# Optimization experiments

Measured on AMD Instinct MI355X. Metric: run time of the kernel, lower is better.

## Reference

```python
import jax, jax.numpy as jnp
import numpy as np

EPS = 1e-12  # torch F.normalize eps


def setup_inputs() -> dict:
    key = jax.random.key(0)
    k1, k2, k3 = jax.random.split(key, 3)
    B, C, N, E, EMB = 128, 16, 128, 4, 16
    OUT = EMB // E  # Linear(emb_sz, emb_sz // num_edges)
    x = jax.random.normal(k1, (B, C, N, EMB), dtype=jnp.float32)
    A = jax.random.uniform(k2, (E, N, N), dtype=jnp.float32)  # non-negative adjacency
    # per-edge-type Linear weights, stored [E, in, out] so y = x @ W[e]
    W = jax.random.normal(k3, (E, EMB, OUT), dtype=jnp.float32) * (1.0 / np.sqrt(EMB))
    return {"x": x, "A": A, "W": W}


def reference(x, A, W):
    # F.normalize(A[e], dim=0): L2-normalize each column -> norm over rows (axis=1 of [E,N,N])
    col_norm = jnp.sqrt(jnp.sum(A * A, axis=1, keepdims=True))  # [E,1,N]
    An = A / jnp.maximum(col_norm, EPS)                         # [E,N,N]
    # x.transpose(3,2) @ An[e] then transpose back:
    # out[e,b,c,m,f] = sum_n x[b,c,n,f] * An[e,n,m]
    msg = jnp.einsum('bcnf,enm->ebcmf', x, An)                  # [E,B,C,N,EMB]
    # per-edge Linear (bias=False) + relu
    h = jax.nn.relu(jnp.einsum('ebcmf,efo->ebcmo', msg, W))     # [E,B,C,N,OUT]
    E_, B, C, N, O = h.shape
    # torch.cat([h_0, h_1, ...], axis=1) -> [B, E*C, N, OUT]
    out = jnp.transpose(h, (1, 0, 2, 3, 4)).reshape(B, E_ * C, N, O)
    return out
```

## Files before the change

kernel.cpp:

```cpp
#include <hip/hip_runtime.h>
#include <math.h>

#define EPSN 1e-12f

typedef __attribute__((ext_vector_type(8))) __bf16 bf16x8;
typedef __attribute__((ext_vector_type(8))) short short8;
typedef __attribute__((ext_vector_type(4))) float floatx4;

static __device__ __forceinline__ unsigned short f2bf(float f) {
    return __builtin_bit_cast(unsigned short, (__bf16)f);
}

__global__ __launch_bounds__(512, 2)
void gcn_one(const float* __restrict__ x, const float* __restrict__ A,
             const float* __restrict__ W, float* __restrict__ out) {
    __shared__ __align__(16) unsigned char xw[32768];
    __shared__ __align__(16) unsigned char at[32768];
    __shared__ float red[16][128];

    const int t   = threadIdx.x;
    const int bc0 = blockIdx.x * 8;
    const int w   = t >> 6;
    const int l   = t & 63;
    const int cl  = l & 15;
    const int lg  = l >> 4;
    const int mw  = w * 16 + cl;
    const int mq  = t & 31;
    const int ng  = t >> 5;

    float4 v4[8];
    #pragma unroll
    for (int j = 0; j < 8; ++j)
        v4[j] = *(const float4*)(A + (size_t)(ng * 8 + j) * 128 + mq * 4);

    bf16x8 bW;
    {
        short8 z = {0, 0, 0, 0, 0, 0, 0, 0};
        bW = __builtin_bit_cast(bf16x8, z);
        if (lg < 2) {
            unsigned short hs[8] __attribute__((aligned(16)));
            #pragma unroll
            for (int j = 0; j < 8; ++j)
                hs[j] = f2bf(W[(cl >> 2) * 64 + (lg * 8 + j) * 4 + (cl & 3)]);
            bW = __builtin_bit_cast(bf16x8, *(const short8*)hs);
        }
    }
    #pragma unroll
    for (int ti = 0; ti < 8; ++ti) {
        int T = w * 8 + ti;
        bf16x8 ax;
        { short8 z = {0, 0, 0, 0, 0, 0, 0, 0}; ax = __builtin_bit_cast(bf16x8, z); }
        if (lg < 2) {
            int R = T * 16 + cl;
            const float* xp = x + ((size_t)bc0 * 128 + R) * 16 + lg * 8;
            float4 a = *(const float4*)xp;
            float4 b = *(const float4*)(xp + 4);
            unsigned short hs[8] __attribute__((aligned(16)));
            hs[0] = f2bf(a.x); hs[1] = f2bf(a.y); hs[2] = f2bf(a.z); hs[3] = f2bf(a.w);
            hs[4] = f2bf(b.x); hs[5] = f2bf(b.y); hs[6] = f2bf(b.z); hs[7] = f2bf(b.w);
            ax = __builtin_bit_cast(bf16x8, *(const short8*)hs);
        }
        floatx4 d = {0.f, 0.f, 0.f, 0.f};
        d = __builtin_amdgcn_mfma_f32_16x16x32_bf16(ax, bW, d, 0, 0, 0);
        int eD = cl >> 2, oD = cl & 3;
        int bcl = T >> 3;
        int nb  = (T & 7) * 16 + lg * 4;
        int r   = bcl * 4 + oD;
        int base = (eD * 32 + r) << 8;
        int s    = (r & 7) << 4;
        #pragma unroll
        for (int q = 0; q < 4; ++q) {
            int off = (base + (nb + q) * 2) ^ s;
            *(unsigned short*)(xw + off) = f2bf(d[q]);
        }
    }

    {
        floatx4 rs = {0.f, 0.f, 0.f, 0.f};
        #pragma unroll
        for (int i = 0; i < 4; ++i) {
            int m = mq * 4 + i;
            unsigned short hs[8] __attribute__((aligned(16)));
            #pragma unroll
            for (int j = 0; j < 8; ++j) {
                float vv = ((const float*)&v4[j])[i];
                rs[i] += vv * vv;
                hs[j] = f2bf(vv);
            }
            int slot = ng ^ (mq & 7);
            *(short8*)(at + ((m << 8) | (slot << 4))) = *(const short8*)hs;
        }
        *(float4*)&red[ng][mq * 4] = *(const float4*)&rs;
    }
    __syncthreads();

    #pragma unroll 1
    for (int e = 0; e < 4; ++e) {
        if (e < 3) {
            const float* An = A + (size_t)(e + 1) * 16384;
            #pragma unroll
            for (int j = 0; j < 8; ++j)
                v4[j] = *(const float4*)(An + (size_t)(ng * 8 + j) * 128 + mq * 4);
        }
        bf16x8 af[2][4];
        #pragma unroll
        for (int rt = 0; rt < 2; ++rt)
            #pragma unroll
            for (int ks = 0; ks < 4; ++ks) {
                int row = rt * 16 + cl;
                int off = (((e * 32 + row) << 8) + (ks * 32 + lg * 8) * 2)
                          ^ ((row & 7) << 4);
                af[rt][ks] = __builtin_bit_cast(bf16x8, *(const short8*)(xw + off));
            }
        bf16x8 bfr[4];
        #pragma unroll
        for (int ks = 0; ks < 4; ++ks) {
            int slot = (ks * 4 + lg) ^ ((mw >> 2) & 7);
            bfr[ks] = __builtin_bit_cast(bf16x8,
                *(const short8*)(at + ((mw << 8) | (slot << 4))));
        }

        floatx4 acc0 = {0.f, 0.f, 0.f, 0.f};
        floatx4 acc1 = {0.f, 0.f, 0.f, 0.f};
        #pragma unroll
        for (int ks = 0; ks < 4; ++ks) {
            acc0 = __builtin_amdgcn_mfma_f32_16x16x32_bf16(af[0][ks], bfr[ks], acc0, 0, 0, 0);
            acc1 = __builtin_amdgcn_mfma_f32_16x16x32_bf16(af[1][ks], bfr[ks], acc1, 0, 0, 0);
        }

        float ssum = 0.f;
        #pragma unroll
        for (int g = 0; g < 16; ++g) ssum += red[g][mw];
        float rn = 1.0f / fmaxf(sqrtf(ssum), EPSN);

        #pragma unroll
        for (int rt = 0; rt < 2; ++rt) {
            floatx4 a = rt ? acc1 : acc0;
            int bc = bc0 + rt * 4 + lg;
            int b = bc >> 4, c = bc & 15;
            float4 o4;
            o4.x = fmaxf(a[0] * rn, 0.f);
            o4.y = fmaxf(a[1] * rn, 0.f);
            o4.z = fmaxf(a[2] * rn, 0.f);
            o4.w = fmaxf(a[3] * rn, 0.f);
            ((float4*)out)[(size_t)(b * 64 + e * 16 + c) * 128 + mw] = o4;
        }
        __syncthreads();
        if (e < 3) {
            floatx4 rs = {0.f, 0.f, 0.f, 0.f};
            #pragma unroll
            for (int i = 0; i < 4; ++i) {
                int m = mq * 4 + i;
                unsigned short hs[8] __attribute__((aligned(16)));
                #pragma unroll
                for (int j = 0; j < 8; ++j) {
                    float vv = ((const float*)&v4[j])[i];
                    rs[i] += vv * vv;
                    hs[j] = f2bf(vv);
                }
                int slot = ng ^ (mq & 7);
                *(short8*)(at + ((m << 8) | (slot << 4))) = *(const short8*)hs;
            }
            *(float4*)&red[ng][mq * 4] = *(const float4*)&rs;
            __syncthreads();
        }
    }
}

extern "C" void kernel_launch(void* const* d_in, const int* in_sizes, int n_in,
                              void* d_out, int out_size, void* d_ws, size_t ws_size,
                              hipStream_t stream) {
    const float* x = (const float*)d_in[0];
    const float* A = (const float*)d_in[1];
    const float* W = (const float*)d_in[2];
    float* out = (float*)d_out;

    gcn_one<<<256, 512, 0, stream>>>(x, A, W, out);
}
```

Measured before the change: 18.96 us.

## Double-buffer normalized adjacency staging in LDS to cut barriers

After: 18.53 us. -2.3%, faster.

```diff
diff --git a/kernel.cpp b/kernel.cpp
--- a/kernel.cpp
+++ b/kernel.cpp
@@ -15,8 +15,8 @@
 void gcn_one(const float* __restrict__ x, const float* __restrict__ A,
              const float* __restrict__ W, float* __restrict__ out) {
     __shared__ __align__(16) unsigned char xw[32768];
-    __shared__ __align__(16) unsigned char at[32768];
-    __shared__ float red[16][128];
+    __shared__ __align__(16) unsigned char at[2][32768];
+    __shared__ float red[2][16][128];
 
     const int t   = threadIdx.x;
     const int bc0 = blockIdx.x * 8;
@@ -28,10 +28,13 @@
     const int mq  = t & 31;
     const int ng  = t >> 5;
 
-    float4 v4[8];
+    float4 v4a[8], v4b[8];
     #pragma unroll
     for (int j = 0; j < 8; ++j)
-        v4[j] = *(const float4*)(A + (size_t)(ng * 8 + j) * 128 + mq * 4);
+        v4a[j] = *(const float4*)(A + (size_t)(ng * 8 + j) * 128 + mq * 4);
+    #pragma unroll
+    for (int j = 0; j < 8; ++j)
+        v4b[j] = *(const float4*)(A + 16384 + (size_t)(ng * 8 + j) * 128 + mq * 4);
 
     bf16x8 bW;
     {
@@ -75,7 +78,7 @@
         }
     }
 
-    {
+    auto stage_write = [&](int buf, const float4* v4) {
         floatx4 rs = {0.f, 0.f, 0.f, 0.f};
         #pragma unroll
         for (int i = 0; i < 4; ++i) {
@@ -88,20 +91,16 @@
                 hs[j] = f2bf(vv);
             }
             int slot = ng ^ (mq & 7);
-            *(short8*)(at + ((m << 8) | (slot << 4))) = *(const short8*)hs;
+            *(short8*)(at[buf] + ((m << 8) | (slot << 4))) = *(const short8*)hs;
         }
-        *(float4*)&red[ng][mq * 4] = *(const float4*)&rs;
-    }
+        *(float4*)&red[buf][ng][mq * 4] = *(const float4*)&rs;
+    };
+
+    stage_write(0, v4a);
+    stage_write(1, v4b);
     __syncthreads();
 
-    #pragma unroll 1
-    for (int e = 0; e < 4; ++e) {
-        if (e < 3) {
-            const float* An = A + (size_t)(e + 1) * 16384;
-            #pragma unroll
-            for (int j = 0; j < 8; ++j)
-                v4[j] = *(const float4*)(An + (size_t)(ng * 8 + j) * 128 + mq * 4);
-        }
+    auto compute_e = [&](int e, int buf) {
         bf16x8 af[2][4];
         #pragma unroll
         for (int rt = 0; rt < 2; ++rt)
@@ -117,9 +116,8 @@
         for (int ks = 0; ks < 4; ++ks) {
             int slot = (ks * 4 + lg) ^ ((mw >> 2) & 7);
             bfr[ks] = __builtin_bit_cast(bf16x8,
-                *(const short8*)(at + ((mw << 8) | (slot << 4))));
+                *(const short8*)(at[buf] + ((mw << 8) | (slot << 4))));
         }
-
         floatx4 acc0 = {0.f, 0.f, 0.f, 0.f};
         floatx4 acc1 = {0.f, 0.f, 0.f, 0.f};
         #pragma unroll
@@ -127,12 +125,10 @@
             acc0 = __builtin_amdgcn_mfma_f32_16x16x32_bf16(af[0][ks], bfr[ks], acc0, 0, 0, 0);
             acc1 = __builtin_amdgcn_mfma_f32_16x16x32_bf16(af[1][ks], bfr[ks], acc1, 0, 0, 0);
         }
-
         float ssum = 0.f;
         #pragma unroll
-        for (int g = 0; g < 16; ++g) ssum += red[g][mw];
+        for (int g = 0; g < 16; ++g) ssum += red[buf][g][mw];
         float rn = 1.0f / fmaxf(sqrtf(ssum), EPSN);
-
         #pragma unroll
         for (int rt = 0; rt < 2; ++rt) {
             floatx4 a = rt ? acc1 : acc0;
@@ -145,26 +141,26 @@
             o4.w = fmaxf(a[3] * rn, 0.f);
             ((float4*)out)[(size_t)(b * 64 + e * 16 + c) * 128 + mw] = o4;
         }
-        __syncthreads();
-        if (e < 3) {
-            floatx4 rs = {0.f, 0.f, 0.f, 0.f};
-            #pragma unroll
-            for (int i = 0; i < 4; ++i) {
-                int m = mq * 4 + i;
-                unsigned short hs[8] __attribute__((aligned(16)));
-                #pragma unroll
-                for (int j = 0; j < 8; ++j) {
-                    float vv = ((const float*)&v4[j])[i];
-                    rs[i] += vv * vv;
-                    hs[j] = f2bf(vv);
-                }
-                int slot = ng ^ (mq & 7);
-                *(short8*)(at + ((m << 8) | (slot << 4))) = *(const short8*)hs;
-            }
-            *(float4*)&red[ng][mq * 4] = *(const float4*)&rs;
-            __syncthreads();
-        }
-    }
+    };
+
+    #pragma unroll
+    for (int j = 0; j < 8; ++j)
+        v4a[j] = *(const float4*)(A + 2 * 16384 + (size_t)(ng * 8 + j) * 128 + mq * 4);
+    compute_e(0, 0);
+    __syncthreads();
+    stage_write(0, v4a);
+
+    #pragma unroll
+    for (int j = 0; j < 8; ++j)
+        v4b[j] = *(const float4*)(A + 3 * 16384 + (size_t)(ng * 8 + j) * 128 + mq * 4);
+    compute_e(1, 1);
+    __syncthreads();
+    stage_write(1, v4b);
+
+    compute_e(2, 0);
+    __syncthreads();
+
+    compute_e(3, 1);
 }
 
 extern "C" void kernel_launch(void* const* d_in, const int* in_sizes, int n_in,
```
